# Optimization experiments

Hardware: AMD Instinct MI355X
Metric: run time of the kernel (lower is better)

## Reference

```python
import jax, jax.numpy as jnp
import numpy as np

TAU = 0.9
TOPK = 8
NUM_LAYERS = 3


def _layer_norm(x, g, b, eps=1e-5):
    mu = jnp.mean(x, axis=-1, keepdims=True)
    var = jnp.var(x, axis=-1, keepdims=True)
    return (x - mu) / jnp.sqrt(var + eps) * g + b


def _forward(x, edge_index, Wi, bi, wp, Wa, ba, ln1_g, ln1_b, ln2_g, ln2_b,
             W1, b1, W2, b2, Wc, bc, Wo, bo):
    N = x.shape[0]
    H = Wi.shape[1]
    # input projection + relu
    x = jax.nn.relu(x @ Wi + bi)
    src, dst = edge_index[0], edge_index[1]
    # ---- priority pi (computed under no_grad, dummy_alpha = 1, x_prev = 0) ----
    delta_x = jnp.sum(jnp.abs(x), axis=1)                      # [N]
    neigh = jax.ops.segment_sum(delta_x[src], dst, num_segments=N)
    pi = jax.lax.stop_gradient(jax.nn.sigmoid(x @ wp + neigh))  # [N]
    # ---- add self loops (selected subgraph == full graph) ----
    loops = jnp.arange(N, dtype=src.dtype)
    src_e = jnp.concatenate([src, loops])
    dst_e = jnp.concatenate([dst, loops])
    Et = src_e.shape[0]
    # ---- edge attention logits: att_mlp(cat[h_i, h_j, p_j]) computed as split matvec ----
    a_dst = x @ Wa[:H]          # contribution of h_i = x[dst]
    a_src = x @ Wa[H:2 * H]     # contribution of h_j = x[src]
    e = a_dst[dst_e] + a_src[src_e] + pi[src_e] * Wa[2 * H] + ba[0]
    e = jax.nn.leaky_relu(e, 0.2) / TAU
    e = jnp.clip(e, -5.0, 5.0)
    exp_e = jnp.exp(e)
    denom = jax.ops.segment_sum(exp_e, dst_e, num_segments=N)
    alpha = exp_e / (denom[dst_e] + 1e-16)
    # ---- per-destination top-k sparsification + renormalization (vectorized) ----
    order = jnp.lexsort((-alpha, dst_e))       # sort by dst, then alpha descending
    dst_s = dst_e[order]
    alpha_s = alpha[order]
    pos = jnp.arange(Et)
    is_new = jnp.concatenate([jnp.ones((1,), bool), dst_s[1:] != dst_s[:-1]])
    grp_start = jax.lax.cummax(jnp.where(is_new, pos, 0))
    rank = pos - grp_start                     # rank within each dst group
    keep = rank < TOPK
    ksum = jax.ops.segment_sum(jnp.where(keep, alpha_s, 0.0), dst_s, num_segments=N)
    alpha_new_s = jnp.where(keep, alpha_s / (ksum[dst_s] + 1e-16), 0.0)
    alpha = jnp.zeros((Et,), x.dtype).at[order].set(alpha_new_s)
    # ---- prenorm blocks with priority-weighted conv (dropout = identity, eval) ----
    h = x
    for l in range(NUM_LAYERS):
        hn = _layer_norm(h, ln1_g[l], ln1_b[l])
        xp = hn @ Wc[l] + bc[l]                               # conv linear
        msg = xp[src_e] * alpha[:, None]                      # [Et, H]
        agg = jax.ops.segment_sum(msg, dst_e, num_segments=N)  # scatter-add
        h = h + jax.nn.relu(agg)
        h2 = _layer_norm(h, ln2_g[l], ln2_b[l])
        h2 = jax.nn.gelu(h2 @ W1[l] + b1[l], approximate=False) @ W2[l] + b2[l]
        h = h + h2
    return h @ Wo + bo


def setup_inputs() -> dict:
    key = jax.random.key(0)
    ks = jax.random.split(key, 10)
    N, E, IN, H, OUT, L, F = 50000, 400000, 256, 256, 64, 3, 512
    def nrm(k, shape, scale):
        return jax.random.normal(k, shape, jnp.float32) * scale
    return {
        "x": nrm(ks[0], (N, IN), 1.0),
        "edge_index": jax.random.randint(ks[1], (2, E), 0, N, dtype=jnp.int32),
        "Wi": nrm(ks[2], (IN, H), IN ** -0.5), "bi": jnp.zeros((H,), jnp.float32),
        "wp": nrm(ks[3], (H,), H ** -0.5),
        "Wa": nrm(ks[4], (2 * H + 1,), (2 * H + 1) ** -0.5), "ba": jnp.zeros((1,), jnp.float32),
        "ln1_g": jnp.ones((L, H), jnp.float32), "ln1_b": jnp.zeros((L, H), jnp.float32),
        "ln2_g": jnp.ones((L, H), jnp.float32), "ln2_b": jnp.zeros((L, H), jnp.float32),
        "W1": nrm(ks[5], (L, H, F), H ** -0.5), "b1": jnp.zeros((L, F), jnp.float32),
        "W2": nrm(ks[6], (L, F, H), F ** -0.5), "b2": jnp.zeros((L, H), jnp.float32),
        "Wc": nrm(ks[7], (L, H, H), H ** -0.5), "bc": jnp.zeros((L, H), jnp.float32),
        "Wo": nrm(ks[8], (H, OUT), H ** -0.5), "bo": jnp.zeros((OUT,), jnp.float32),
    }


def reference(x, edge_index, Wi, bi, wp, Wa, ba, ln1_g, ln1_b, ln2_g, ln2_b,
              W1, b1, W2, b2, Wc, bc, Wo, bo):
    return _forward(x, edge_index, Wi, bi, wp, Wa, ba, ln1_g, ln1_b, ln2_g, ln2_b,
                    W1, b1, W2, b2, Wc, bc, Wo, bo)
```

## Files before the change

### kernel.cpp

```cpp
#include <hip/hip_runtime.h>
#include <math.h>

#define TAUF 0.9f

typedef unsigned int u32;
typedef unsigned short ushort;
typedef __attribute__((ext_vector_type(8))) short short8;
typedef __attribute__((ext_vector_type(8))) _Float16 half8;
typedef __attribute__((ext_vector_type(4))) float f32x4;
typedef __attribute__((ext_vector_type(4))) unsigned short us4;
typedef __attribute__((ext_vector_type(8))) unsigned short us8;

__device__ __forceinline__ ushort f2bf(float f) {
  u32 u = __builtin_bit_cast(u32, f);
  u32 r = (u + 0x7FFFu + ((u >> 16) & 1u)) >> 16;
  return (ushort)r;
}
__device__ __forceinline__ float bf2f(ushort s) {
  u32 u = ((u32)s) << 16;
  return __builtin_bit_cast(float, u);
}

__device__ __forceinline__ float gelu_f(float x) {
  float z = x * 0.70710678118654752f;
  float az = fabsf(z);
  float t = 1.f / fmaf(0.3275911f, az, 1.f);
  float poly = t * fmaf(t, fmaf(t, fmaf(t, fmaf(t, 1.061405429f, -1.453152027f),
                                        1.421413741f), -0.284496736f), 0.254829592f);
  float erfa = fmaf(-poly, __expf(-az * az), 1.f);
  float s = (z < 0.f) ? -erfa : erfa;
  return 0.5f * x * (1.f + s);
}

__device__ __forceinline__ void gload16(const void* g, void* l) {
  __builtin_amdgcn_global_load_lds(
      (const __attribute__((address_space(1))) u32*)g,
      (__attribute__((address_space(3))) u32*)l, 16, 0, 0);
}

__launch_bounds__(256, 2)
__global__ void gemm_in_mfma(const float* __restrict__ X,
                             const _Float16* __restrict__ Bh, const _Float16* __restrict__ Bl,
                             const float* __restrict__ bias, const float* __restrict__ Wa,
                             const float* __restrict__ wp, const float* __restrict__ g1,
                             const float* __restrict__ b1g, ushort* __restrict__ hb,
                             ushort* __restrict__ hn, float* __restrict__ delta,
                             float* __restrict__ adst, float* __restrict__ asrc,
                             float* __restrict__ xwp, int M) {
  __shared__ char lds[81920];
  char* As_h = lds;
  char* As_l = lds + 8192;
  char* Bs_h = lds + 16384;
  char* Bs_l = lds + 49152;
  const int tid = threadIdx.x;
  const int wave = tid >> 6, lane = tid & 63;
  const int bm = blockIdx.x * 64;

  const int arow = tid >> 2;
  const int ac4 = tid & 3;
  const int aoff0 = arow * 128 + (((2 * ac4 + 0) ^ (arow & 7)) << 4);
  const int aoff1 = arow * 128 + (((2 * ac4 + 1) ^ (arow & 7)) << 4);
  const int srow = lane >> 3;
  const int scol = (((lane & 7) ^ srow) << 3);

  f32x4 accH[4][4], accC[4][4];
#pragma unroll
  for (int i = 0; i < 4; ++i)
#pragma unroll
    for (int j = 0; j < 4; ++j) {
      accH[i][j] = (f32x4){0.f, 0.f, 0.f, 0.f};
      accC[i][j] = (f32x4){0.f, 0.f, 0.f, 0.f};
    }

  int ar = bm + arow;
  ar = (ar < M) ? ar : (M - 1);
  const float* xrow = X + (size_t)ar * 256 + ac4 * 16;

#pragma unroll
  for (int k0 = 0; k0 < 256; k0 += 64) {
    float4 x0 = *reinterpret_cast<const float4*>(xrow + k0);
    float4 x1 = *reinterpret_cast<const float4*>(xrow + k0 + 4);
    float4 x2 = *reinterpret_cast<const float4*>(xrow + k0 + 8);
    float4 x3 = *reinterpret_cast<const float4*>(xrow + k0 + 12);
    float xs[16] = {x0.x, x0.y, x0.z, x0.w, x1.x, x1.y, x1.z, x1.w,
                    x2.x, x2.y, x2.z, x2.w, x3.x, x3.y, x3.z, x3.w};
    half8 hh0, hh1, ll0, ll1;
#pragma unroll
    for (int j = 0; j < 8; ++j) {
      _Float16 hv = (_Float16)xs[j];
      hh0[j] = hv;
      ll0[j] = (_Float16)((xs[j] - (float)hv) * 2048.f);
      _Float16 hv2 = (_Float16)xs[8 + j];
      hh1[j] = hv2;
      ll1[j] = (_Float16)((xs[8 + j] - (float)hv2) * 2048.f);
    }
    *reinterpret_cast<half8*>(As_h + aoff0) = hh0;
    *reinterpret_cast<half8*>(As_h + aoff1) = hh1;
    *reinterpret_cast<half8*>(As_l + aoff0) = ll0;
    *reinterpret_cast<half8*>(As_l + aoff1) = ll1;
#pragma unroll
    for (int r = 0; r < 8; ++r) {
      const int ch = r * 4 + wave;
      const int br = ch * 8 + srow;
      gload16(Bh + (size_t)br * 256 + k0 + scol, Bs_h + ch * 1024);
      gload16(Bl + (size_t)br * 256 + k0 + scol, Bs_l + ch * 1024);
    }
    __syncthreads();
#pragma unroll
    for (int kk = 0; kk < 2; ++kk) {
      const int c = (kk * 32 + (lane >> 4) * 8) * 2;
      half8 ah[4], al[4];
#pragma unroll
      for (int mi = 0; mi < 4; ++mi) {
        const int rr = mi * 16 + (lane & 15);
        const int off = rr * 128 + (c ^ ((rr & 7) << 4));
        ah[mi] = *(const half8*)(As_h + off);
        al[mi] = *(const half8*)(As_l + off);
      }
#pragma unroll
      for (int ni = 0; ni < 4; ++ni) {
        const int rr = wave * 64 + ni * 16 + (lane & 15);
        half8 bh = *(const half8*)(Bs_h + rr * 128 + (c ^ ((rr & 7) << 4)));
#pragma unroll
        for (int mi = 0; mi < 4; ++mi)
          accH[mi][ni] = __builtin_amdgcn_mfma_f32_16x16x32_f16(ah[mi], bh,
                                                                accH[mi][ni], 0, 0, 0);
#pragma unroll
        for (int mi = 0; mi < 4; ++mi)
          accC[mi][ni] = __builtin_amdgcn_mfma_f32_16x16x32_f16(al[mi], bh,
                                                                accC[mi][ni], 0, 0, 0);
      }
#pragma unroll
      for (int ni = 0; ni < 4; ++ni) {
        const int rr = wave * 64 + ni * 16 + (lane & 15);
        half8 bl = *(const half8*)(Bs_l + rr * 128 + (c ^ ((rr & 7) << 4)));
#pragma unroll
        for (int mi = 0; mi < 4; ++mi)
          accC[mi][ni] = __builtin_amdgcn_mfma_f32_16x16x32_f16(ah[mi], bl,
                                                                accC[mi][ni], 0, 0, 0);
      }
    }
    __syncthreads();
  }

  float bb[4], wa0[4], wa1[4], wpv[4], gg[4], gb[4];
#pragma unroll
  for (int ni = 0; ni < 4; ++ni) {
    const int c = wave * 64 + ni * 16 + (lane & 15);
    bb[ni] = bias[c]; wa0[ni] = Wa[c]; wa1[ni] = Wa[256 + c];
    wpv[ni] = wp[c]; gg[ni] = g1[c]; gb[ni] = b1g[c];
  }
  float* red = (float*)lds;
  float* muA = (float*)(lds + 5120);
  float* isA = (float*)(lds + 5376);
  const float inv = 1.f / 2048.f;
#pragma unroll
  for (int mi = 0; mi < 4; ++mi) {
#pragma unroll
    for (int reg = 0; reg < 4; ++reg) {
      const int lrow = mi * 16 + (lane >> 4) * 4 + reg;
      const int row = bm + lrow;
      float v[4];
      float p0 = 0.f, p1 = 0.f, p2 = 0.f, p3 = 0.f, p4 = 0.f;
#pragma unroll
      for (int ni = 0; ni < 4; ++ni) {
        float t = accH[mi][ni][reg] + accC[mi][ni][reg] * inv + bb[ni];
        t = fmaxf(t, 0.f);
        v[ni] = t;
        p0 += t; p1 += t * wa0[ni]; p2 += t * wa1[ni]; p3 += t * wpv[ni];
        p4 += t * t;
      }
      if (row < M) {
#pragma unroll
        for (int ni = 0; ni < 4; ++ni)
          hb[(size_t)row * 256 + wave * 64 + ni * 16 + (lane & 15)] = f2bf(v[ni]);
      }
#pragma unroll
      for (int ni = 0; ni < 4; ++ni) accH[mi][ni][reg] = v[ni];
#pragma unroll
      for (int off = 1; off < 16; off <<= 1) {
        p0 += __shfl_xor(p0, off, 64);
        p1 += __shfl_xor(p1, off, 64);
        p2 += __shfl_xor(p2, off, 64);
        p3 += __shfl_xor(p3, off, 64);
        p4 += __shfl_xor(p4, off, 64);
      }
      if ((lane & 15) == 0) {
        red[(0 * 4 + wave) * 64 + lrow] = p0;
        red[(1 * 4 + wave) * 64 + lrow] = p1;
        red[(2 * 4 + wave) * 64 + lrow] = p2;
        red[(3 * 4 + wave) * 64 + lrow] = p3;
        red[(4 * 4 + wave) * 64 + lrow] = p4;
      }
    }
  }
  __syncthreads();
  if (tid < 64) {
    float s0 = 0.f, s1 = 0.f, s2 = 0.f, s3 = 0.f, s4 = 0.f;
#pragma unroll
    for (int w = 0; w < 4; ++w) {
      s0 += red[(0 * 4 + w) * 64 + tid];
      s1 += red[(1 * 4 + w) * 64 + tid];
      s2 += red[(2 * 4 + w) * 64 + tid];
      s3 += red[(3 * 4 + w) * 64 + tid];
      s4 += red[(4 * 4 + w) * 64 + tid];
    }
    const int row = bm + tid;
    if (row < M) {
      delta[row] = s0; adst[row] = s1; asrc[row] = s2; xwp[row] = s3;
    }
    float mu = s0 * (1.f / 256.f);
    muA[tid] = mu;
    isA[tid] = rsqrtf(s4 * (1.f / 256.f) - mu * mu + 1e-5f);
  }
  __syncthreads();
#pragma unroll
  for (int mi = 0; mi < 4; ++mi) {
#pragma unroll
    for (int reg = 0; reg < 4; ++reg) {
      const int lrow = mi * 16 + (lane >> 4) * 4 + reg;
      const int row = bm + lrow;
      if (row >= M) continue;
      const float mu = muA[lrow], is = isA[lrow];
#pragma unroll
      for (int ni = 0; ni < 4; ++ni) {
        const int col = wave * 64 + ni * 16 + (lane & 15);
        hn[(size_t)row * 256 + col] = f2bf((accH[mi][ni][reg] - mu) * is * gg[ni] + gb[ni]);
      }
    }
  }
}

__global__ void gather_k(const ushort* __restrict__ hn, const int* __restrict__ ksrc,
                         const float* __restrict__ kw, ushort* __restrict__ hagg, int N) {
  int d = blockIdx.x * 8 + (threadIdx.x >> 5);
  if (d >= N) return;
  int sub = threadIdx.x & 31;
  us8 xv[8];
  float w[8];
#pragma unroll
  for (int j = 0; j < 8; ++j) {
    int s = ksrc[(size_t)d * 8 + j];
    w[j] = kw[(size_t)d * 8 + j];
    xv[j] = *reinterpret_cast<const us8*>(hn + (size_t)s * 256 + sub * 8);
  }
  float a[8] = {0.f, 0.f, 0.f, 0.f, 0.f, 0.f, 0.f, 0.f};
#pragma unroll
  for (int j = 0; j < 8; ++j)
#pragma unroll
    for (int q = 0; q < 8; ++q) a[q] += w[j] * bf2f(xv[j][q]);
  us8 o;
#pragma unroll
  for (int q = 0; q < 8; ++q) o[q] = f2bf(a[q]);
  *reinterpret_cast<us8*>(hagg + (size_t)d * 256 + sub * 8) = o;
}

__launch_bounds__(512, 4)
__global__ void gemm_conv_aggln(const ushort* __restrict__ A, const ushort* __restrict__ Bt,
                                const float* __restrict__ bias, const float* __restrict__ g2,
                                const float* __restrict__ b2g, ushort* __restrict__ hb,
                                ushort* __restrict__ hn, int M) {
  __shared__ ushort As[128 * 64];
  __shared__ ushort Bs[256 * 64];
  const int tid = threadIdx.x;
  const int wave = tid >> 6, lane = tid & 63;
  const int bm = blockIdx.x * 128;
  const int wm = (wave >> 2) * 64, wn = (wave & 3) * 64;
  const int srow = lane >> 3;
  const int scol = (((lane & 7) ^ srow) << 3);

  f32x4 acc[4][4];
#pragma unroll
  for (int i = 0; i < 4; ++i)
#pragma unroll
    for (int j = 0; j < 4; ++j) acc[i][j] = (f32x4){0.f, 0.f, 0.f, 0.f};

  for (int k0 = 0; k0 < 256; k0 += 64) {
#pragma unroll
    for (int r = 0; r < 2; ++r) {
      const int ch = r * 8 + wave;
      int ar = bm + ch * 8 + srow;
      ar = (ar < M) ? ar : (M - 1);
      gload16(A + (size_t)ar * 256 + k0 + scol, (char*)As + ch * 1024);
    }
#pragma unroll
    for (int r = 0; r < 4; ++r) {
      const int ch = r * 8 + wave;
      const int br = ch * 8 + srow;
      gload16(Bt + (size_t)br * 256 + k0 + scol, (char*)Bs + ch * 1024);
    }
    __syncthreads();
#pragma unroll
    for (int kk = 0; kk < 2; ++kk) {
      const int c = (kk * 32 + (lane >> 4) * 8) * 2;
      short8 a[4];
#pragma unroll
      for (int mi = 0; mi < 4; ++mi) {
        const int rr = wm + mi * 16 + (lane & 15);
        a[mi] = *(const short8*)((const char*)As + rr * 128 + (c ^ ((rr & 7) << 4)));
      }
#pragma unroll
      for (int ni = 0; ni < 4; ++ni) {
        const int rr = wn + ni * 16 + (lane & 15);
        short8 b = *(const short8*)((const char*)Bs + rr * 128 + (c ^ ((rr & 7) << 4)));
#pragma unroll
        for (int mi = 0; mi < 4; ++mi)
          acc[mi][ni] = __builtin_amdgcn_mfma_f32_16x16x32_bf16(a[mi], b,
                                                                acc[mi][ni], 0, 0, 0);
      }
    }
    __syncthreads();
  }

  float bb[4];
#pragma unroll
  for (int ni = 0; ni < 4; ++ni) bb[ni] = bias[wn + ni * 16 + (lane & 15)];

  float* redS = (float*)As;
  float* redQ = redS + 512;
  float* muA  = redQ + 512;
  float* isA  = muA + 128;

#pragma unroll
  for (int mi = 0; mi < 4; ++mi) {
#pragma unroll
    for (int reg = 0; reg < 4; ++reg) {
      const int lrow = wm + mi * 16 + (lane >> 4) * 4 + reg;
      const int row = bm + lrow;
      const bool ok = (row < M);
      float pS = 0.f, pQ = 0.f;
#pragma unroll
      for (int ni = 0; ni < 4; ++ni) {
        const int col = wn + ni * 16 + (lane & 15);
        float t = fmaxf(acc[mi][ni][reg] + bb[ni], 0.f);
        if (ok) {
          t += bf2f(hb[(size_t)row * 256 + col]);
          hb[(size_t)row * 256 + col] = f2bf(t);
        }
        acc[mi][ni][reg] = t;
        pS += t;
        pQ += t * t;
      }
#pragma unroll
      for (int off = 1; off < 16; off <<= 1) {
        pS += __shfl_xor(pS, off, 64);
        pQ += __shfl_xor(pQ, off, 64);
      }
      if ((lane & 15) == 0) {
        redS[(wave & 3) * 128 + lrow] = pS;
        redQ[(wave & 3) * 128 + lrow] = pQ;
      }
    }
  }
  __syncthreads();
  if (tid < 128) {
    float S = redS[tid] + redS[128 + tid] + redS[256 + tid] + redS[384 + tid];
    float Q = redQ[tid] + redQ[128 + tid] + redQ[256 + tid] + redQ[384 + tid];
    float mu = S * (1.f / 256.f);
    muA[tid] = mu;
    isA[tid] = rsqrtf(Q * (1.f / 256.f) - mu * mu + 1e-5f);
  }
  __syncthreads();
  float gg[4], gb[4];
#pragma unroll
  for (int ni = 0; ni < 4; ++ni) {
    gg[ni] = g2[wn + ni * 16 + (lane & 15)];
    gb[ni] = b2g[wn + ni * 16 + (lane & 15)];
  }
#pragma unroll
  for (int mi = 0; mi < 4; ++mi) {
#pragma unroll
    for (int reg = 0; reg < 4; ++reg) {
      const int lrow = wm + mi * 16 + (lane >> 4) * 4 + reg;
      const int row = bm + lrow;
      if (row >= M) continue;
      const float mu = muA[lrow], is = isA[lrow];
#pragma unroll
      for (int ni = 0; ni < 4; ++ni) {
        const int col = wn + ni * 16 + (lane & 15);
        hn[(size_t)row * 256 + col] = f2bf((acc[mi][ni][reg] - mu) * is * gg[ni] + gb[ni]);
      }
    }
  }
}

__launch_bounds__(512, 4)
__global__ void gemm_ffn1(const ushort* __restrict__ A, const ushort* __restrict__ Bt,
                          const float* __restrict__ bias, ushort* __restrict__ u, int M) {
  __shared__ ushort As[128 * 64];
  __shared__ ushort Bs[256 * 64];
  const int tid = threadIdx.x;
  const int wave = tid >> 6, lane = tid & 63;
  const int bm = blockIdx.x * 128;
  const int bn = blockIdx.y * 256;
  const int wm = (wave >> 2) * 64, wn = (wave & 3) * 64;
  const int srow = lane >> 3;
  const int scol = (((lane & 7) ^ srow) << 3);

  f32x4 acc[4][4];
#pragma unroll
  for (int i = 0; i < 4; ++i)
#pragma unroll
    for (int j = 0; j < 4; ++j) acc[i][j] = (f32x4){0.f, 0.f, 0.f, 0.f};

  for (int k0 = 0; k0 < 256; k0 += 64) {
#pragma unroll
    for (int r = 0; r < 2; ++r) {
      const int ch = r * 8 + wave;
      int ar = bm + ch * 8 + srow;
      ar = (ar < M) ? ar : (M - 1);
      gload16(A + (size_t)ar * 256 + k0 + scol, (char*)As + ch * 1024);
    }
#pragma unroll
    for (int r = 0; r < 4; ++r) {
      const int ch = r * 8 + wave;
      const int br = bn + ch * 8 + srow;
      gload16(Bt + (size_t)br * 256 + k0 + scol, (char*)Bs + ch * 1024);
    }
    __syncthreads();
#pragma unroll
    for (int kk = 0; kk < 2; ++kk) {
      const int c = (kk * 32 + (lane >> 4) * 8) * 2;
      short8 a[4];
#pragma unroll
      for (int mi = 0; mi < 4; ++mi) {
        const int rr = wm + mi * 16 + (lane & 15);
        a[mi] = *(const short8*)((const char*)As + rr * 128 + (c ^ ((rr & 7) << 4)));
      }
#pragma unroll
      for (int ni = 0; ni < 4; ++ni) {
        const int rr = wn + ni * 16 + (lane & 15);
        short8 b = *(const short8*)((const char*)Bs + rr * 128 + (c ^ ((rr & 7) << 4)));
#pragma unroll
        for (int mi = 0; mi < 4; ++mi)
          acc[mi][ni] = __builtin_amdgcn_mfma_f32_16x16x32_bf16(a[mi], b,
                                                                acc[mi][ni], 0, 0, 0);
      }
    }
    __syncthreads();
  }

  float bb[4];
#pragma unroll
  for (int ni = 0; ni < 4; ++ni) bb[ni] = bias[bn + wn + ni * 16 + (lane & 15)];
#pragma unroll
  for (int mi = 0; mi < 4; ++mi) {
#pragma unroll
    for (int reg = 0; reg < 4; ++reg) {
      const int row = bm + wm + mi * 16 + (lane >> 4) * 4 + reg;
      if (row >= M) continue;
#pragma unroll
      for (int ni = 0; ni < 4; ++ni) {
        const int col = bn + wn + ni * 16 + (lane & 15);
        u[(size_t)row * 512 + col] = f2bf(gelu_f(acc[mi][ni][reg] + bb[ni]));
      }
    }
  }
}

template <int LAST>
__launch_bounds__(512, 4)
__global__ void gemm_ffn2ln(const ushort* __restrict__ A, const ushort* __restrict__ Bt,
                            const float* __restrict__ bias, const float* __restrict__ g1,
                            const float* __restrict__ b1g, ushort* __restrict__ hb,
                            ushort* __restrict__ hn, int M) {
  __shared__ ushort As[128 * 64];
  __shared__ ushort Bs[256 * 64];
  const int tid = threadIdx.x;
  const int wave = tid >> 6, lane = tid & 63;
  const int bm = blockIdx.x * 128;
  const int wm = (wave >> 2) * 64, wn = (wave & 3) * 64;
  const int srow = lane >> 3;
  const int scol = (((lane & 7) ^ srow) << 3);

  f32x4 acc[4][4];
#pragma unroll
  for (int i = 0; i < 4; ++i)
#pragma unroll
    for (int j = 0; j < 4; ++j) acc[i][j] = (f32x4){0.f, 0.f, 0.f, 0.f};

  for (int k0 = 0; k0 < 512; k0 += 64) {
#pragma unroll
    for (int r = 0; r < 2; ++r) {
      const int ch = r * 8 + wave;
      int ar = bm + ch * 8 + srow;
      ar = (ar < M) ? ar : (M - 1);
      gload16(A + (size_t)ar * 512 + k0 + scol, (char*)As + ch * 1024);
    }
#pragma unroll
    for (int r = 0; r < 4; ++r) {
      const int ch = r * 8 + wave;
      const int br = ch * 8 + srow;
      gload16(Bt + (size_t)br * 512 + k0 + scol, (char*)Bs + ch * 1024);
    }
    __syncthreads();
#pragma unroll
    for (int kk = 0; kk < 2; ++kk) {
      const int c = (kk * 32 + (lane >> 4) * 8) * 2;
      short8 a[4];
#pragma unroll
      for (int mi = 0; mi < 4; ++mi) {
        const int rr = wm + mi * 16 + (lane & 15);
        a[mi] = *(const short8*)((const char*)As + rr * 128 + (c ^ ((rr & 7) << 4)));
      }
#pragma unroll
      for (int ni = 0; ni < 4; ++ni) {
        const int rr = wn + ni * 16 + (lane & 15);
        short8 b = *(const short8*)((const char*)Bs + rr * 128 + (c ^ ((rr & 7) << 4)));
#pragma unroll
        for (int mi = 0; mi < 4; ++mi)
          acc[mi][ni] = __builtin_amdgcn_mfma_f32_16x16x32_bf16(a[mi], b,
                                                                acc[mi][ni], 0, 0, 0);
      }
    }
    __syncthreads();
  }

  float bb[4];
#pragma unroll
  for (int ni = 0; ni < 4; ++ni) bb[ni] = bias[wn + ni * 16 + (lane & 15)];

  float* redS = (float*)As;
  float* redQ = redS + 512;
  float* muA  = redQ + 512;
  float* isA  = muA + 128;

#pragma unroll
  for (int mi = 0; mi < 4; ++mi) {
#pragma unroll
    for (int reg = 0; reg < 4; ++reg) {
      const int lrow = wm + mi * 16 + (lane >> 4) * 4 + reg;
      const int row = bm + lrow;
      const bool ok = (row < M);
      float pS = 0.f, pQ = 0.f;
#pragma unroll
      for (int ni = 0; ni < 4; ++ni) {
        const int col = wn + ni * 16 + (lane & 15);
        float t = acc[mi][ni][reg] + bb[ni];
        if (ok) t += bf2f(hb[(size_t)row * 256 + col]);
        acc[mi][ni][reg] = t;
        if (LAST) {
          if (ok) hn[(size_t)row * 256 + col] = f2bf(t);
        } else {
          if (ok) hb[(size_t)row * 256 + col] = f2bf(t);
          pS += t;
          pQ += t * t;
        }
      }
      if (!LAST) {
#pragma unroll
        for (int off = 1; off < 16; off <<= 1) {
          pS += __shfl_xor(pS, off, 64);
          pQ += __shfl_xor(pQ, off, 64);
        }
        if ((lane & 15) == 0) {
          redS[(wave & 3) * 128 + lrow] = pS;
          redQ[(wave & 3) * 128 + lrow] = pQ;
        }
      }
    }
  }
  if (LAST) return;
  __syncthreads();
  if (tid < 128) {
    float S = redS[tid] + redS[128 + tid] + redS[256 + tid] + redS[384 + tid];
    float Q = redQ[tid] + redQ[128 + tid] + redQ[256 + tid] + redQ[384 + tid];
    float mu = S * (1.f / 256.f);
    muA[tid] = mu;
    isA[tid] = rsqrtf(Q * (1.f / 256.f) - mu * mu + 1e-5f);
  }
  __syncthreads();
  float gg[4], gb[4];
#pragma unroll
  for (int ni = 0; ni < 4; ++ni) {
    gg[ni] = g1[wn + ni * 16 + (lane & 15)];
    gb[ni] = b1g[wn + ni * 16 + (lane & 15)];
  }
#pragma unroll
  for (int mi = 0; mi < 4; ++mi) {
#pragma unroll
    for (int reg = 0; reg < 4; ++reg) {
      const int lrow = wm + mi * 16 + (lane >> 4) * 4 + reg;
      const int row = bm + lrow;
      if (row >= M) continue;
      const float mu = muA[lrow], is = isA[lrow];
#pragma unroll
      for (int ni = 0; ni < 4; ++ni) {
        const int col = wn + ni * 16 + (lane & 15);
        hn[(size_t)row * 256 + col] = f2bf((acc[mi][ni][reg] - mu) * is * gg[ni] + gb[ni]);
      }
    }
  }
}

__launch_bounds__(256)
__global__ void gemm_out(const ushort* __restrict__ A, const ushort* __restrict__ Bt,
                         const float* __restrict__ bias, float* __restrict__ C, int M) {
  __shared__ ushort As[128 * 64];
  __shared__ ushort Bs[64 * 64];
  const int tid = threadIdx.x;
  const int wave = tid >> 6, lane = tid & 63;
  const int bm = blockIdx.x * 128;
  const int wm = wave * 32;
  const int srow = lane >> 3;
  const int scol = (((lane & 7) ^ srow) << 3);
  f32x4 acc[2][4];
#pragma unroll
  for (int i = 0; i < 2; ++i)
#pragma unroll
    for (int j = 0; j < 4; ++j) acc[i][j] = (f32x4){0.f, 0.f, 0.f, 0.f};

  for (int k0 = 0; k0 < 256; k0 += 64) {
#pragma unroll
    for (int r = 0; r < 4; ++r) {
      const int ch = r * 4 + wave;
      int ar = bm + ch * 8 + srow;
      ar = (ar < M) ? ar : (M - 1);
      gload16(A + (size_t)ar * 256 + k0 + scol, (char*)As + ch * 1024);
    }
#pragma unroll
    for (int r = 0; r < 2; ++r) {
      const int ch = r * 4 + wave;
      const int br = ch * 8 + srow;
      gload16(Bt + (size_t)br * 256 + k0 + scol, (char*)Bs + ch * 1024);
    }
    __syncthreads();
#pragma unroll
    for (int kk = 0; kk < 2; ++kk) {
      const int c = (kk * 32 + (lane >> 4) * 8) * 2;
      short8 a[2], b[4];
#pragma unroll
      for (int mi = 0; mi < 2; ++mi) {
        const int rr = wm + mi * 16 + (lane & 15);
        a[mi] = *(const short8*)((const char*)As + rr * 128 + (c ^ ((rr & 7) << 4)));
      }
#pragma unroll
      for (int ni = 0; ni < 4; ++ni) {
        const int rr = ni * 16 + (lane & 15);
        b[ni] = *(const short8*)((const char*)Bs + rr * 128 + (c ^ ((rr & 7) << 4)));
      }
#pragma unroll
      for (int mi = 0; mi < 2; ++mi)
#pragma unroll
        for (int ni = 0; ni < 4; ++ni)
          acc[mi][ni] = __builtin_amdgcn_mfma_f32_16x16x32_bf16(a[mi], b[ni],
                                                                acc[mi][ni], 0, 0, 0);
    }
    __syncthreads();
  }
  float bb[4];
#pragma unroll
  for (int ni = 0; ni < 4; ++ni) bb[ni] = bias[ni * 16 + (lane & 15)];
#pragma unroll
  for (int mi = 0; mi < 2; ++mi) {
#pragma unroll
    for (int reg = 0; reg < 4; ++reg) {
      const int row = bm + wm + mi * 16 + (lane >> 4) * 4 + reg;
      if (row >= M) continue;
#pragma unroll
      for (int ni = 0; ni < 4; ++ni) {
        const int col = ni * 16 + (lane & 15);
        C[(size_t)row * 64 + col] = acc[mi][ni][reg] + bb[ni];
      }
    }
  }
}

#define W_IN 65536
#define W_TOTAL (196608 + 393216 + 393216 + 16384)
__global__ void prep_k(const float* __restrict__ Wi, const float* __restrict__ Wc,
                       const float* __restrict__ W1, const float* __restrict__ W2,
                       const float* __restrict__ Wo, _Float16* __restrict__ WiTh,
                       _Float16* __restrict__ WiTl, ushort* __restrict__ WcT,
                       ushort* __restrict__ W1T, ushort* __restrict__ W2T,
                       ushort* __restrict__ WoT, float* __restrict__ zbase, int zn) {
  int i = blockIdx.x * 256 + threadIdx.x;
  if (i < W_IN) {
    int n = i >> 8, k = i & 255;
    float w = Wi[(size_t)k * 256 + n];
    _Float16 hv = (_Float16)w;
    WiTh[i] = hv;
    WiTl[i] = (_Float16)((w - (float)hv) * 2048.f);
  } else if ((i -= W_IN) < W_TOTAL) {
    int j = i;
    if (j < 196608) {
      int l = j / 65536, r = j % 65536, n = r >> 8, k = r & 255;
      WcT[j] = f2bf(Wc[(size_t)l * 65536 + k * 256 + n]);
    } else if ((j -= 196608) < 393216) {
      int l = j / 131072, r = j % 131072, n = r >> 8, k = r & 255;
      W1T[j] = f2bf(W1[(size_t)l * 131072 + k * 512 + n]);
    } else if ((j -= 393216) < 393216) {
      int l = j / 131072, r = j % 131072, n = r >> 9, k = r & 511;
      W2T[j] = f2bf(W2[(size_t)l * 131072 + k * 256 + n]);
    } else {
      j -= 393216;
      int n = j >> 8, k = j & 255;
      WoT[j] = f2bf(Wo[k * 64 + n]);
    }
  } else {
    int z = i - W_TOTAL;
    if (z < zn) zbase[z] = 0.f;
  }
}

__global__ void neigh_k(const int* __restrict__ src, const int* __restrict__ dst,
                        const float* __restrict__ delta, float* __restrict__ neigh, int E) {
  int e = blockIdx.x * 256 + threadIdx.x;
  if (e < E) atomicAdd(&neigh[dst[e]], delta[src[e]]);
}

__global__ void logits_k(const int* __restrict__ src, const int* __restrict__ dst,
                         const float* __restrict__ adst, const float* __restrict__ asrc,
                         const float* __restrict__ xwp, const float* __restrict__ neigh,
                         const float* __restrict__ Wa, const float* __restrict__ ba,
                         float* __restrict__ expe, float* __restrict__ denom,
                         int* __restrict__ cnt, int* __restrict__ slots,
                         int E, int Et, int N) {
  int e = blockIdx.x * 256 + threadIdx.x;
  if (e >= Et) return;
  int s, d;
  if (e < E) { s = src[e]; d = dst[e]; } else { s = e - E; d = s; }
  float pis = 1.f / (1.f + expf(-(xwp[s] + neigh[s])));
  float v = adst[d] + asrc[s] + pis * Wa[512] + ba[0];
  v = (v >= 0.f ? v : 0.2f * v) / TAUF;
  v = fminf(fmaxf(v, -5.f), 5.f);
  float ex = expf(v);
  expe[e] = ex;
  atomicAdd(&denom[d], ex);
  int p = atomicAdd(&cnt[d], 1);
  if (p < 64) slots[(size_t)p * N + d] = e;
}

__device__ __forceinline__ bool better(float a, int e, float a2, int e2) {
  return a > a2 || (a == a2 && e < e2);
}

__global__ void topk_k(const int* __restrict__ cnt, const int* __restrict__ slots,
                       const float* __restrict__ expe, const float* __restrict__ denom,
                       const int* __restrict__ src, int* __restrict__ ksrc,
                       float* __restrict__ kw, int N, int E) {
  int d = blockIdx.x * 256 + threadIdx.x;
  if (d >= N) return;
  int deg = min(cnt[d], 64);
  float D = denom[d] + 1e-16f;
  float av[8]; int ai[8]; int kc = 0;
  for (int t = 0; t < deg; ++t) {
    int e = slots[(size_t)t * N + d];
    float a = expe[e] / D;
    if (kc < 8) {
      int p = kc++;
      while (p > 0 && better(a, e, av[p - 1], ai[p - 1])) {
        av[p] = av[p - 1]; ai[p] = ai[p - 1]; --p;
      }
      av[p] = a; ai[p] = e;
    } else if (better(a, e, av[7], ai[7])) {
      int p = 7;
      while (p > 0 && better(a, e, av[p - 1], ai[p - 1])) {
        av[p] = av[p - 1]; ai[p] = ai[p - 1]; --p;
      }
      av[p] = a; ai[p] = e;
    }
  }
  float ks = 0.f;
  for (int j = 0; j < kc; ++j) ks += av[j];
  float inv = 1.f / (ks + 1e-16f);
#pragma unroll
  for (int j = 0; j < 8; ++j) {
    if (j < kc) {
      int e = ai[j];
      ksrc[(size_t)d * 8 + j] = (e < E) ? src[e] : (e - E);
      kw[(size_t)d * 8 + j] = av[j] * inv;
    } else {
      ksrc[(size_t)d * 8 + j] = 0;
      kw[(size_t)d * 8 + j] = 0.f;
    }
  }
}

extern "C" void kernel_launch(void* const* d_in, const int* in_sizes, int n_in,
                              void* d_out, int out_size, void* d_ws, size_t ws_size,
                              hipStream_t stream) {
  const float* X   = (const float*)d_in[0];
  const int*   EI  = (const int*)d_in[1];
  const float* Wi  = (const float*)d_in[2];
  const float* bi  = (const float*)d_in[3];
  const float* wp  = (const float*)d_in[4];
  const float* Wa  = (const float*)d_in[5];
  const float* ba  = (const float*)d_in[6];
  const float* l1g = (const float*)d_in[7];
  const float* l1b = (const float*)d_in[8];
  const float* l2g = (const float*)d_in[9];
  const float* l2b = (const float*)d_in[10];
  const float* W1  = (const float*)d_in[11];
  const float* b1  = (const float*)d_in[12];
  const float* W2  = (const float*)d_in[13];
  const float* b2  = (const float*)d_in[14];
  const float* Wc  = (const float*)d_in[15];
  const float* bc  = (const float*)d_in[16];
  const float* Wo  = (const float*)d_in[17];
  const float* bo  = (const float*)d_in[18];

  const int N = in_sizes[0] / 256;
  const int E = in_sizes[1] / 2;
  const int Et = E + N;
  const int* srcp = EI;
  const int* dstp = EI + E;

  float* ws = (float*)d_ws;
  size_t off = 0;
  auto alloc = [&](size_t n) { float* p = ws + off; off += n; return p; };
  const size_t NH = (size_t)N * 256;
  ushort* hb   = (ushort*)alloc(NH / 2);
  ushort* hn   = (ushort*)alloc(NH / 2);
  ushort* hagg = (ushort*)alloc(NH / 2);
  ushort* u    = (ushort*)alloc(NH);
  _Float16* WiTh = (_Float16*)alloc(65536 / 2);
  _Float16* WiTl = (_Float16*)alloc(65536 / 2);
  ushort* WcT  = (ushort*)alloc(3 * 65536 / 2);
  ushort* W1T  = (ushort*)alloc(3 * 131072 / 2);
  ushort* W2T  = (ushort*)alloc(3 * 131072 / 2);
  ushort* WoT  = (ushort*)alloc(16384 / 2);
  float* delta = alloc(N);
  float* adst  = alloc(N);
  float* asrc  = alloc(N);
  float* xwp   = alloc(N);
  float* expe  = alloc(Et);
  float* neigh = alloc(N);
  float* denom = alloc(N);
  int*   cnt   = (int*)alloc(N);
  int*   slots = (int*)alloc((size_t)N * 64);
  int*   ksrc  = (int*)alloc((size_t)N * 8);
  float* kw    = alloc((size_t)N * 8);

  prep_k<<<(W_IN + W_TOTAL + 3 * N + 255) / 256, 256, 0, stream>>>(
      Wi, Wc, W1, W2, Wo, WiTh, WiTl, WcT, W1T, W2T, WoT, neigh, 3 * N);

  gemm_in_mfma<<<(N + 63) / 64, 256, 0, stream>>>(
      X, WiTh, WiTl, bi, Wa, wp, l1g, l1b, hb, hn,
      delta, adst, asrc, xwp, N);
  neigh_k<<<(E + 255) / 256, 256, 0, stream>>>(srcp, dstp, delta, neigh, E);
  logits_k<<<(Et + 255) / 256, 256, 0, stream>>>(srcp, dstp, adst, asrc, xwp, neigh,
                                                 Wa, ba, expe, denom, cnt, slots,
                                                 E, Et, N);
  topk_k<<<(N + 255) / 256, 256, 0, stream>>>(cnt, slots, expe, denom, srcp,
                                              ksrc, kw, N, E);

  const int GM = (N + 127) / 128;
  for (int l = 0; l < 3; ++l) {
    gather_k<<<(N + 7) / 8, 256, 0, stream>>>(hn, ksrc, kw, hagg, N);
    gemm_conv_aggln<<<GM, 512, 0, stream>>>(
        hagg, WcT + (size_t)l * 65536, bc + l * 256,
        l2g + l * 256, l2b + l * 256, hb, hn, N);
    gemm_ffn1<<<dim3(GM, 2), 512, 0, stream>>>(
        hn, W1T + (size_t)l * 131072, b1 + l * 512, u, N);
    if (l < 2)
      gemm_ffn2ln<0><<<GM, 512, 0, stream>>>(
          u, W2T + (size_t)l * 131072, b2 + l * 256,
          l1g + (l + 1) * 256, l1b + (l + 1) * 256, hb, hn, N);
    else
      gemm_ffn2ln<1><<<GM, 512, 0, stream>>>(
          u, W2T + (size_t)l * 131072, b2 + l * 256,
          nullptr, nullptr, hb, hn, N);
  }
  gemm_out<<<(N + 127) / 128, 256, 0, stream>>>(hn, WoT, bo, (float*)d_out, N);
}
```

Before: 610.4 us.

## Fuse FFN up- and down-projection GEMMs, keeping GELU intermediate in LDS

Merges the two FFN kernels into one. Each block computes the up-projection plus GELU in 64-column chunks, stores each chunk swizzled in shared memory, and immediately accumulates it into the down-projection, with the residual and LayerNorm epilogue unchanged. The aim is to remove the global write and re-read of the N×512 intermediate and one launch per layer. In exchange, the hn tile is reloaded from L2 for every chunk, the first-stage MFMA tiles are small with many barriers, shared memory use grows to 64KB per block, and the grid is halved. The input and output hn pointers now alias despite both being marked __restrict__.

```diff
diff --git a/kernel.cpp b/kernel.cpp
--- a/kernel.cpp
+++ b/kernel.cpp
@@ -384,38 +384,93 @@
   }
 }
 
+template <int LAST>
 __launch_bounds__(512, 4)
-__global__ void gemm_ffn1(const ushort* __restrict__ A, const ushort* __restrict__ Bt,
-                          const float* __restrict__ bias, ushort* __restrict__ u, int M) {
-  __shared__ ushort As[128 * 64];
+__global__ void gemm_ffn(const ushort* __restrict__ hn, const ushort* __restrict__ W1T,
+                         const float* __restrict__ b1, const ushort* __restrict__ W2T,
+                         const float* __restrict__ b2, const float* __restrict__ g1,
+                         const float* __restrict__ b1g, ushort* __restrict__ hb,
+                         ushort* __restrict__ hn_out, int M) {
+  __shared__ ushort Hs[128 * 64];
   __shared__ ushort Bs[256 * 64];
+  __shared__ ushort Uq[128 * 64];
   const int tid = threadIdx.x;
   const int wave = tid >> 6, lane = tid & 63;
   const int bm = blockIdx.x * 128;
-  const int bn = blockIdx.y * 256;
-  const int wm = (wave >> 2) * 64, wn = (wave & 3) * 64;
+  const int wm1 = (wave >> 2) * 32, wn1 = (wave & 3) * 32;
+  const int wm2 = (wave >> 2) * 64, wn2 = (wave & 3) * 64;
   const int srow = lane >> 3;
   const int scol = (((lane & 7) ^ srow) << 3);
 
-  f32x4 acc[4][4];
+  f32x4 acc2[4][4];
 #pragma unroll
   for (int i = 0; i < 4; ++i)
 #pragma unroll
-    for (int j = 0; j < 4; ++j) acc[i][j] = (f32x4){0.f, 0.f, 0.f, 0.f};
-
-  for (int k0 = 0; k0 < 256; k0 += 64) {
-#pragma unroll
-    for (int r = 0; r < 2; ++r) {
-      const int ch = r * 8 + wave;
-      int ar = bm + ch * 8 + srow;
-      ar = (ar < M) ? ar : (M - 1);
-      gload16(A + (size_t)ar * 256 + k0 + scol, (char*)As + ch * 1024);
+    for (int j = 0; j < 4; ++j) acc2[i][j] = (f32x4){0.f, 0.f, 0.f, 0.f};
+
+  for (int e = 0; e < 8; ++e) {
+    const int E = e * 64;
+    f32x4 acc1[2][2];
+#pragma unroll
+    for (int i = 0; i < 2; ++i)
+#pragma unroll
+      for (int j = 0; j < 2; ++j) acc1[i][j] = (f32x4){0.f, 0.f, 0.f, 0.f};
+
+    for (int ks = 0; ks < 4; ++ks) {
+      const int k0 = ks * 64;
+#pragma unroll
+      for (int r = 0; r < 2; ++r) {
+        const int ch = r * 8 + wave;
+        int ar = bm + ch * 8 + srow;
+        ar = (ar < M) ? ar : (M - 1);
+        gload16(hn + (size_t)ar * 256 + k0 + scol, (char*)Hs + ch * 1024);
+      }
+      {
+        const int ur = E + wave * 8 + srow;
+        gload16(W1T + (size_t)ur * 256 + k0 + scol, (char*)Bs + wave * 1024);
+      }
+      __syncthreads();
+#pragma unroll
+      for (int kk = 0; kk < 2; ++kk) {
+        const int c = (kk * 32 + (lane >> 4) * 8) * 2;
+        short8 bfrag[2];
+#pragma unroll
+        for (int ni = 0; ni < 2; ++ni) {
+          const int rr = wn1 + ni * 16 + (lane & 15);
+          bfrag[ni] = *(const short8*)((const char*)Hs + rr * 128 + (c ^ ((rr & 7) << 4)));
+        }
+#pragma unroll
+        for (int mi = 0; mi < 2; ++mi) {
+          const int rr = wm1 + mi * 16 + (lane & 15);
+          short8 a = *(const short8*)((const char*)Bs + rr * 128 + (c ^ ((rr & 7) << 4)));
+#pragma unroll
+          for (int ni = 0; ni < 2; ++ni)
+            acc1[mi][ni] = __builtin_amdgcn_mfma_f32_16x16x32_bf16(a, bfrag[ni],
+                                                                   acc1[mi][ni], 0, 0, 0);
+        }
+      }
+      __syncthreads();
+    }
+#pragma unroll
+    for (int mi = 0; mi < 2; ++mi) {
+#pragma unroll
+      for (int ni = 0; ni < 2; ++ni) {
+        const int ucb = wm1 + mi * 16 + (lane >> 4) * 4;
+        const int hrow = wn1 + ni * 16 + (lane & 15);
+        us4 pk;
+#pragma unroll
+        for (int reg = 0; reg < 4; ++reg)
+          pk[reg] = f2bf(gelu_f(acc1[mi][ni][reg] + b1[E + ucb + reg]));
+        const int slot = ucb >> 3, half = (ucb >> 2) & 1;
+        *reinterpret_cast<us4*>((char*)Uq + hrow * 128 +
+                                ((slot ^ (hrow & 7)) << 4) + half * 8) = pk;
+      }
     }
 #pragma unroll
     for (int r = 0; r < 4; ++r) {
       const int ch = r * 8 + wave;
-      const int br = bn + ch * 8 + srow;
-      gload16(Bt + (size_t)br * 256 + k0 + scol, (char*)Bs + ch * 1024);
+      const int oc = ch * 8 + srow;
+      gload16(W2T + (size_t)oc * 512 + E + scol, (char*)Bs + ch * 1024);
     }
     __syncthreads();
 #pragma unroll
@@ -424,17 +479,18 @@
       short8 a[4];
 #pragma unroll
       for (int mi = 0; mi < 4; ++mi) {
-        const int rr = wm + mi * 16 + (lane & 15);
-        a[mi] = *(const short8*)((const char*)As + rr * 128 + (c ^ ((rr & 7) << 4)));
-      }
-#pragma unroll
-      for (int ni = 0; ni < 4; ++ni) {
-        const int rr = wn + ni * 16 + (lane & 15);
+        const int rr = wm2 + mi * 16 + (lane & 15);
+        const int slot = kk * 4 + (lane >> 4);
+        a[mi] = *(const short8*)((const char*)Uq + rr * 128 + ((slot ^ (rr & 7)) << 4));
+      }
+#pragma unroll
+      for (int ni = 0; ni < 4; ++ni) {
+        const int rr = wn2 + ni * 16 + (lane & 15);
         short8 b = *(const short8*)((const char*)Bs + rr * 128 + (c ^ ((rr & 7) << 4)));
 #pragma unroll
         for (int mi = 0; mi < 4; ++mi)
-          acc[mi][ni] = __builtin_amdgcn_mfma_f32_16x16x32_bf16(a[mi], b,
-                                                                acc[mi][ni], 0, 0, 0);
+          acc2[mi][ni] = __builtin_amdgcn_mfma_f32_16x16x32_bf16(a[mi], b,
+                                                                 acc2[mi][ni], 0, 0, 0);
       }
     }
     __syncthreads();
@@ -442,85 +498,9 @@
 
   float bb[4];
 #pragma unroll
-  for (int ni = 0; ni < 4; ++ni) bb[ni] = bias[bn + wn + ni * 16 + (lane & 15)];
-#pragma unroll
-  for (int mi = 0; mi < 4; ++mi) {
-#pragma unroll
-    for (int reg = 0; reg < 4; ++reg) {
-      const int row = bm + wm + mi * 16 + (lane >> 4) * 4 + reg;
-      if (row >= M) continue;
-#pragma unroll
-      for (int ni = 0; ni < 4; ++ni) {
-        const int col = bn + wn + ni * 16 + (lane & 15);
-        u[(size_t)row * 512 + col] = f2bf(gelu_f(acc[mi][ni][reg] + bb[ni]));
-      }
-    }
-  }
-}
-
-template <int LAST>
-__launch_bounds__(512, 4)
-__global__ void gemm_ffn2ln(const ushort* __restrict__ A, const ushort* __restrict__ Bt,
-                            const float* __restrict__ bias, const float* __restrict__ g1,
-                            const float* __restrict__ b1g, ushort* __restrict__ hb,
-                            ushort* __restrict__ hn, int M) {
-  __shared__ ushort As[128 * 64];
-  __shared__ ushort Bs[256 * 64];
-  const int tid = threadIdx.x;
-  const int wave = tid >> 6, lane = tid & 63;
-  const int bm = blockIdx.x * 128;
-  const int wm = (wave >> 2) * 64, wn = (wave & 3) * 64;
-  const int srow = lane >> 3;
-  const int scol = (((lane & 7) ^ srow) << 3);
-
-  f32x4 acc[4][4];
-#pragma unroll
-  for (int i = 0; i < 4; ++i)
-#pragma unroll
-    for (int j = 0; j < 4; ++j) acc[i][j] = (f32x4){0.f, 0.f, 0.f, 0.f};
-
-  for (int k0 = 0; k0 < 512; k0 += 64) {
-#pragma unroll
-    for (int r = 0; r < 2; ++r) {
-      const int ch = r * 8 + wave;
-      int ar = bm + ch * 8 + srow;
-      ar = (ar < M) ? ar : (M - 1);
-      gload16(A + (size_t)ar * 512 + k0 + scol, (char*)As + ch * 1024);
-    }
-#pragma unroll
-    for (int r = 0; r < 4; ++r) {
-      const int ch = r * 8 + wave;
-      const int br = ch * 8 + srow;
-      gload16(Bt + (size_t)br * 512 + k0 + scol, (char*)Bs + ch * 1024);
-    }
-    __syncthreads();
-#pragma unroll
-    for (int kk = 0; kk < 2; ++kk) {
-      const int c = (kk * 32 + (lane >> 4) * 8) * 2;
-      short8 a[4];
-#pragma unroll
-      for (int mi = 0; mi < 4; ++mi) {
-        const int rr = wm + mi * 16 + (lane & 15);
-        a[mi] = *(const short8*)((const char*)As + rr * 128 + (c ^ ((rr & 7) << 4)));
-      }
-#pragma unroll
-      for (int ni = 0; ni < 4; ++ni) {
-        const int rr = wn + ni * 16 + (lane & 15);
-        short8 b = *(const short8*)((const char*)Bs + rr * 128 + (c ^ ((rr & 7) << 4)));
-#pragma unroll
-        for (int mi = 0; mi < 4; ++mi)
-          acc[mi][ni] = __builtin_amdgcn_mfma_f32_16x16x32_bf16(a[mi], b,
-                                                                acc[mi][ni], 0, 0, 0);
-      }
-    }
-    __syncthreads();
-  }
-
-  float bb[4];
-#pragma unroll
-  for (int ni = 0; ni < 4; ++ni) bb[ni] = bias[wn + ni * 16 + (lane & 15)];
-
-  float* redS = (float*)As;
+  for (int ni = 0; ni < 4; ++ni) bb[ni] = b2[wn2 + ni * 16 + (lane & 15)];
+
+  float* redS = (float*)Hs;
   float* redQ = redS + 512;
   float* muA  = redQ + 512;
   float* isA  = muA + 128;
@@ -529,18 +509,18 @@
   for (int mi = 0; mi < 4; ++mi) {
 #pragma unroll
     for (int reg = 0; reg < 4; ++reg) {
-      const int lrow = wm + mi * 16 + (lane >> 4) * 4 + reg;
+      const int lrow = wm2 + mi * 16 + (lane >> 4) * 4 + reg;
       const int row = bm + lrow;
       const bool ok = (row < M);
       float pS = 0.f, pQ = 0.f;
 #pragma unroll
       for (int ni = 0; ni < 4; ++ni) {
-        const int col = wn + ni * 16 + (lane & 15);
-        float t = acc[mi][ni][reg] + bb[ni];
+        const int col = wn2 + ni * 16 + (lane & 15);
+        float t = acc2[mi][ni][reg] + bb[ni];
         if (ok) t += bf2f(hb[(size_t)row * 256 + col]);
-        acc[mi][ni][reg] = t;
+        acc2[mi][ni][reg] = t;
         if (LAST) {
-          if (ok) hn[(size_t)row * 256 + col] = f2bf(t);
+          if (ok) hn_out[(size_t)row * 256 + col] = f2bf(t);
         } else {
           if (ok) hb[(size_t)row * 256 + col] = f2bf(t);
           pS += t;
@@ -573,21 +553,21 @@
   float gg[4], gb[4];
 #pragma unroll
   for (int ni = 0; ni < 4; ++ni) {
-    gg[ni] = g1[wn + ni * 16 + (lane & 15)];
-    gb[ni] = b1g[wn + ni * 16 + (lane & 15)];
+    gg[ni] = g1[wn2 + ni * 16 + (lane & 15)];
+    gb[ni] = b1g[wn2 + ni * 16 + (lane & 15)];
   }
 #pragma unroll
   for (int mi = 0; mi < 4; ++mi) {
 #pragma unroll
     for (int reg = 0; reg < 4; ++reg) {
-      const int lrow = wm + mi * 16 + (lane >> 4) * 4 + reg;
+      const int lrow = wm2 + mi * 16 + (lane >> 4) * 4 + reg;
       const int row = bm + lrow;
       if (row >= M) continue;
       const float mu = muA[lrow], is = isA[lrow];
 #pragma unroll
       for (int ni = 0; ni < 4; ++ni) {
-        const int col = wn + ni * 16 + (lane & 15);
-        hn[(size_t)row * 256 + col] = f2bf((acc[mi][ni][reg] - mu) * is * gg[ni] + gb[ni]);
+        const int col = wn2 + ni * 16 + (lane & 15);
+        hn_out[(size_t)row * 256 + col] = f2bf((acc2[mi][ni][reg] - mu) * is * gg[ni] + gb[ni]);
       }
     }
   }
@@ -813,7 +793,6 @@
   ushort* hb   = (ushort*)alloc(NH / 2);
   ushort* hn   = (ushort*)alloc(NH / 2);
   ushort* hagg = (ushort*)alloc(NH / 2);
-  ushort* u    = (ushort*)alloc(NH);
   _Float16* WiTh = (_Float16*)alloc(65536 / 2);
   _Float16* WiTl = (_Float16*)alloc(65536 / 2);
   ushort* WcT  = (ushort*)alloc(3 * 65536 / 2);
@@ -851,15 +830,15 @@
     gemm_conv_aggln<<<GM, 512, 0, stream>>>(
         hagg, WcT + (size_t)l * 65536, bc + l * 256,
         l2g + l * 256, l2b + l * 256, hb, hn, N);
-    gemm_ffn1<<<dim3(GM, 2), 512, 0, stream>>>(
-        hn, W1T + (size_t)l * 131072, b1 + l * 512, u, N);
     if (l < 2)
-      gemm_ffn2ln<0><<<GM, 512, 0, stream>>>(
-          u, W2T + (size_t)l * 131072, b2 + l * 256,
+      gemm_ffn<0><<<GM, 512, 0, stream>>>(
+          hn, W1T + (size_t)l * 131072, b1 + l * 512,
+          W2T + (size_t)l * 131072, b2 + l * 256,
           l1g + (l + 1) * 256, l1b + (l + 1) * 256, hb, hn, N);
     else
-      gemm_ffn2ln<1><<<GM, 512, 0, stream>>>(
-          u, W2T + (size_t)l * 131072, b2 + l * 256,
+      gemm_ffn<1><<<GM, 512, 0, stream>>>(
+          hn, W1T + (size_t)l * 131072, b1 + l * 512,
+          W2T + (size_t)l * 131072, b2 + l * 256,
           nullptr, nullptr, hb, hn, N);
   }
   gemm_out<<<(N + 127) / 128, 256, 0, stream>>>(hn, WoT, bo, (float*)d_out, N);
```

Result: slower. 656.1 us (+7.5%).
